# Performance work log

Hardware: AMD Instinct MI355X
Metric: run time of the kernel (lower is better)

## Reference

```python
import jax, jax.numpy as jnp
import numpy as np

N = 1024
NEVAL = 131072
NUM_POLES = 8
DOMAIN = (-1.0, 1.0)
DOMAIN_LEN = DOMAIN[1] - DOMAIN[0]
EPS = 1e-14


def _cheb_nodes(n):
    # Chebyshev points of the second kind: cos(pi * linspace(0, 1, n))
    return jnp.cos(jnp.pi * jnp.linspace(0.0, 1.0, n))


def _to_standard(x):
    return 2.0 * (x - DOMAIN[0]) / DOMAIN_LEN - 1.0


def _barycentric_weights(nodes, poles_real, poles_imag):
    # Vectorized equivalent of the original per-node Python loop.
    n = nodes.shape[0]
    diff = nodes[:, None] - nodes[None, :]            # (N, N)
    eye = jnp.eye(n, dtype=bool)
    # log_weights[j] = -sum_{i!=j} log|nodes[j]-nodes[i]|
    log_w = -jnp.sum(jnp.log(jnp.where(eye, 1.0, jnp.abs(diff))), axis=1)
    # signs[j] = (-1)^(# of negative off-diagonal diffs); diagonal diff==0 contributes nothing
    neg_count = jnp.sum(diff < 0, axis=1)
    signs = jnp.where(neg_count % 2 == 0, 1.0, -1.0)
    # each conjugate pole pair contributes 2*log(sqrt((x-r)^2 + i^2)) = log((x-r)^2 + i^2)
    pole_term = jnp.log((nodes[:, None] - poles_real[None, :]) ** 2
                        + poles_imag[None, :] ** 2)   # (N, M)
    log_w = log_w + jnp.sum(pole_term, axis=1)
    log_w = log_w - jnp.max(log_w)
    w = signs * jnp.exp(log_w)
    return w / jnp.abs(w[0])


def setup_inputs() -> dict:
    key = jax.random.key(0)
    k1, k2, k3, k4 = jax.random.split(key, 4)
    x_eval = jax.random.uniform(k1, (NEVAL,), dtype=jnp.float32)  # in [0,1) subset of domain
    values = jax.random.normal(k2, (N,), dtype=jnp.float32)
    poles_real = jax.random.normal(k3, (NUM_POLES,), dtype=jnp.float32)
    poles_imag = jax.random.normal(k4, (NUM_POLES,), dtype=jnp.float32)
    return {"x_eval": x_eval, "values": values,
            "poles_real": poles_real, "poles_imag": poles_imag}


def reference(x_eval, values, poles_real, poles_imag):
    nodes = _cheb_nodes(N)
    nodes_std = _to_standard(nodes)                   # identity for domain (-1,1)
    w = _barycentric_weights(nodes, poles_real, poles_imag)

    x_std = _to_standard(x_eval)
    d_x = x_std[None, :] - nodes_std[:, None]         # (N, NEVAL)
    small = jnp.abs(d_x) < EPS
    small_any = jnp.any(small, axis=0)                # (NEVAL,)
    d_safe = jnp.where(small, 1.0, d_x)
    inv = jnp.where(small_any[None, :], 0.0, 1.0 / d_safe)
    inv = jnp.where(small, 1.0, inv)                  # exact-hit columns: indicator row -> 1

    num = jnp.einsum('n,nm,n->m', values, inv, w)
    den = jnp.einsum('nm,n->m', inv, w)
    return num / den
```

## Files before the change

kernel.cpp:

```cpp
#include <hip/hip_runtime.h>
#include <math.h>

#define N_NODES 1024
#define N_EVAL 131072
#define NUM_POLES 8
#define PI_D 3.14159265358979323846

__global__ __launch_bounds__(512, 4) void eval_kernel(
    const float* __restrict__ x_eval,
    const float* __restrict__ values,
    const float* __restrict__ poles_real,
    const float* __restrict__ poles_imag,
    float* __restrict__ out) {
    __shared__ __align__(16) float s_n[N_NODES];
    __shared__ __align__(16) float s_w[N_NODES];
    __shared__ __align__(16) float s_v[N_NODES];
    __shared__ float2 s_r[8][256];

    const int t = threadIdx.x;

#pragma unroll
    for (int h = 0; h < 2; ++h) {
        const int j = t + h * 512;
        const double nd = cos(PI_D * (double)j / (double)(N_NODES - 1));
        double prod = (j == 0 || j == N_NODES - 1) ? 0.5 : 1.0;
#pragma unroll
        for (int m = 0; m < NUM_POLES; ++m) {
            const double dr = nd - (double)poles_real[m];
            const double di = (double)poles_imag[m];
            prod *= dr * dr + di * di;
        }
        if (j & 1) prod = -prod;
        s_n[j] = (float)nd;
        s_w[j] = (float)prod;
        s_v[j] = (float)(prod * (double)values[j]);
    }
    __syncthreads();

    const int lane = t & 63;
    const int wid  = t >> 6;
    const int pbase = blockIdx.x * 256;
    const float x0 = x_eval[pbase + lane];
    const float x1 = x_eval[pbase + 64 + lane];
    const float x2 = x_eval[pbase + 128 + lane];
    const float x3 = x_eval[pbase + 192 + lane];

    const float4* n4 = (const float4*)s_n + wid * 32;
    const float4* w4 = (const float4*)s_w + wid * 32;
    const float4* v4 = (const float4*)s_v + wid * 32;

    float a0 = 0.0f, b0 = 0.0f, a1 = 0.0f, b1 = 0.0f;
    float a2 = 0.0f, b2 = 0.0f, a3 = 0.0f, b3 = 0.0f;

#define NODE(C)                                                            \
    {                                                                      \
        const float d0 = x0 - an.C;                                        \
        const float d1 = x1 - an.C;                                        \
        const float d2 = x2 - an.C;                                        \
        const float d3 = x3 - an.C;                                        \
        const float r0 = __builtin_amdgcn_rcpf(d0);                        \
        const float r1 = __builtin_amdgcn_rcpf(d1);                        \
        const float r2 = __builtin_amdgcn_rcpf(d2);                        \
        const float r3 = __builtin_amdgcn_rcpf(d3);                        \
        a0 = fmaf(av.C, r0, a0); b0 = fmaf(aw.C, r0, b0);                  \
        a1 = fmaf(av.C, r1, a1); b1 = fmaf(aw.C, r1, b1);                  \
        a2 = fmaf(av.C, r2, a2); b2 = fmaf(aw.C, r2, b2);                  \
        a3 = fmaf(av.C, r3, a3); b3 = fmaf(aw.C, r3, b3);                  \
    }

#pragma unroll 4
    for (int q = 0; q < 32; ++q) {
        const float4 an = n4[q];
        const float4 aw = w4[q];
        const float4 av = v4[q];
        NODE(x) NODE(y) NODE(z) NODE(w)
    }
#undef NODE

    s_r[wid][lane]       = make_float2(a0, b0);
    s_r[wid][lane + 64]  = make_float2(a1, b1);
    s_r[wid][lane + 128] = make_float2(a2, b2);
    s_r[wid][lane + 192] = make_float2(a3, b3);
    __syncthreads();

    if (t < 256) {
        float nn = 0.0f, dd = 0.0f;
#pragma unroll
        for (int w = 0; w < 8; ++w) {
            const float2 pr = s_r[w][t];
            nn += pr.x;
            dd += pr.y;
        }
        float res = nn / dd;
        if (__builtin_expect(__builtin_isnan(res), 0)) {
            const float x = x_eval[pbase + t];
            float hn = 0.0f, hd = 0.0f;
            for (int j = 0; j < N_NODES; ++j) {
                if (s_n[j] == x) { hn += s_v[j]; hd += s_w[j]; }
            }
            res = hn / hd;
        }
        out[pbase + t] = res;
    }
}

extern "C" void kernel_launch(void* const* d_in, const int* in_sizes, int n_in,
                              void* d_out, int out_size, void* d_ws, size_t ws_size,
                              hipStream_t stream) {
    const float* x_eval     = (const float*)d_in[0];
    const float* values     = (const float*)d_in[1];
    const float* poles_real = (const float*)d_in[2];
    const float* poles_imag = (const float*)d_in[3];
    float* out = (float*)d_out;

    eval_kernel<<<N_EVAL / 256, 512, 0, stream>>>(x_eval, values,
                                                  poles_real, poles_imag, out);
}
```

Before: 128.0 us.

## Split weight setup into separate kernel and stream node data via scalar loads

Barycentric weights and nodes are now computed once by a small setup kernel into workspace, rather than redundantly in every block with double-precision cos. The eval kernel uses a wave-uniform node slice so node, weight and value reads become scalar loads, and each thread evaluates one point instead of four. This removes per-block setup work and LDS traffic, at the cost of an extra launch and less per-thread reuse of each node load. The original fused kernel is kept as a fallback when no workspace is provided.

```diff
diff --git a/kernel.cpp b/kernel.cpp
--- a/kernel.cpp
+++ b/kernel.cpp
@@ -6,7 +6,92 @@
 #define NUM_POLES 8
 #define PI_D 3.14159265358979323846
 
-__global__ __launch_bounds__(512, 4) void eval_kernel(
+
+__global__ __launch_bounds__(256) void setup_kernel(
+    const float* __restrict__ values,
+    const float* __restrict__ poles_real,
+    const float* __restrict__ poles_imag,
+    float* __restrict__ ws) {
+    const int j = blockIdx.x * 256 + threadIdx.x;
+    const double nd = cos(PI_D * (double)j / (double)(N_NODES - 1));
+    double prod = (j == 0 || j == N_NODES - 1) ? 0.5 : 1.0;
+#pragma unroll
+    for (int m = 0; m < NUM_POLES; ++m) {
+        const double dr = nd - (double)poles_real[m];
+        const double di = (double)poles_imag[m];
+        prod *= dr * dr + di * di;
+    }
+    if (j & 1) prod = -prod;
+    ws[j]        = (float)nd;
+    ws[j + 1024] = (float)prod;
+    ws[j + 2048] = (float)(prod * (double)values[j]);
+}
+
+__global__ __launch_bounds__(256, 8) void eval_scalar_kernel(
+    const float* __restrict__ x_eval,
+    const float* __restrict__ ws,
+    float* __restrict__ out) {
+    __shared__ float2 s_red[4][64];
+
+    const int t = threadIdx.x;
+    const int lane = t & 63;
+    const int wid = __builtin_amdgcn_readfirstlane(t >> 6);
+    const int pbase = blockIdx.x * 64;
+
+    const float x = x_eval[pbase + lane];
+
+    const float* __restrict__ nn = ws + wid * 256;
+    const float* __restrict__ wq = ws + 1024 + wid * 256;
+    const float* __restrict__ vq = ws + 2048 + wid * 256;
+
+    float a0 = 0.0f, b0 = 0.0f, a1 = 0.0f, b1 = 0.0f;
+
+#pragma unroll 2
+    for (int j = 0; j < 256; j += 8) {
+#pragma unroll
+        for (int k = 0; k < 8; k += 2) {
+            const float n0 = nn[j + k];
+            const float w0 = wq[j + k];
+            const float v0 = vq[j + k];
+            const float n1 = nn[j + k + 1];
+            const float w1 = wq[j + k + 1];
+            const float v1 = vq[j + k + 1];
+            const float d0 = x - n0;
+            const float d1 = x - n1;
+            const float r0 = __builtin_amdgcn_rcpf(d0);
+            const float r1 = __builtin_amdgcn_rcpf(d1);
+            a0 = fmaf(v0, r0, a0);
+            b0 = fmaf(w0, r0, b0);
+            a1 = fmaf(v1, r1, a1);
+            b1 = fmaf(w1, r1, b1);
+        }
+    }
+
+    s_red[wid][lane] = make_float2(a0 + a1, b0 + b1);
+    __syncthreads();
+
+    if (t < 64) {
+        float num = 0.0f, den = 0.0f;
+#pragma unroll
+        for (int w = 0; w < 4; ++w) {
+            const float2 p = s_red[w][t];
+            num += p.x;
+            den += p.y;
+        }
+        float res = num / den;
+        if (__builtin_expect(__builtin_isnan(res), 0)) {
+            const float xx = x_eval[pbase + t];
+            float hn = 0.0f, hd = 0.0f;
+            for (int jj = 0; jj < N_NODES; ++jj) {
+                if (ws[jj] == xx) { hn += ws[2048 + jj]; hd += ws[1024 + jj]; }
+            }
+            res = hn / hd;
+        }
+        out[pbase + t] = res;
+    }
+}
+
+__global__ __launch_bounds__(512, 4) void eval_kernel_fused(
     const float* __restrict__ x_eval,
     const float* __restrict__ values,
     const float* __restrict__ poles_real,
@@ -113,6 +198,13 @@
     const float* poles_imag = (const float*)d_in[3];
     float* out = (float*)d_out;
 
-    eval_kernel<<<N_EVAL / 256, 512, 0, stream>>>(x_eval, values,
-                                                  poles_real, poles_imag, out);
-}
+    if (ws_size >= 3 * N_NODES * sizeof(float)) {
+        float* ws = (float*)d_ws;
+        setup_kernel<<<N_NODES / 256, 256, 0, stream>>>(values, poles_real,
+                                                        poles_imag, ws);
+        eval_scalar_kernel<<<N_EVAL / 64, 256, 0, stream>>>(x_eval, ws, out);
+    } else {
+        eval_kernel_fused<<<N_EVAL / 256, 512, 0, stream>>>(
+            x_eval, values, poles_real, poles_imag, out);
+    }
+}
```

Measured after the change: 116.4 us, median of 2. -9.0%, faster.
